# Kernel optimization log

Measured on AMD Instinct MI355X. Metric: run time of the kernel, lower is better.

The kernel has to match this reference:

```python
import jax, jax.numpy as jnp
import numpy as np

ENC_LEN, B, ENC2, DEC, E = 1024, 64, 1024, 512, 512

def setup_inputs() -> dict:
    key = jax.random.key(0)
    k1, k2, k3, k4 = jax.random.split(key, 4)
    enc_output = jax.random.normal(k1, (ENC_LEN, B, ENC2), dtype=jnp.float32)
    s = jax.random.normal(k2, (1, B, DEC), dtype=jnp.float32)
    # torch Linear weights: [out_features, in_features], no bias
    W_attn = jax.random.normal(k3, (E, ENC2 + DEC), dtype=jnp.float32) * (1.0 / np.sqrt(ENC2 + DEC))
    W_v = jax.random.normal(k4, (1, E), dtype=jnp.float32) * (1.0 / np.sqrt(E))
    return {"enc_output": enc_output, "s": s, "W_attn": W_attn, "W_v": W_v}

def reference(enc_output, s, W_attn, W_v):
    # cat([enc_output, s.repeat(L,1,1)], -1) @ W_attn.T  ==  enc @ Wa_e.T + s @ Wa_s.T (broadcast)
    enc2 = enc_output.shape[-1]
    Wa_e = W_attn[:, :enc2]          # [E, 2*enc_hid]
    Wa_s = W_attn[:, enc2:]          # [E, dec_hid]
    pre = jnp.einsum('lbc,ec->lbe', enc_output, Wa_e) + jnp.einsum('obd,ed->obe', s, Wa_s)
    engry = jnp.tanh(pre)            # [L, B, E]
    attention = jnp.einsum('lbe,oe->lbo', engry, W_v)[..., 0].T  # [B, L]
    return jax.nn.softmax(attention, axis=-1)
```

## Files before the change

### kernel.cpp

```cpp
#include <hip/hip_runtime.h>
#include <hip/hip_bf16.h>
#include <stdint.h>

typedef __bf16 bf16;
typedef __bf16 bf16x4 __attribute__((ext_vector_type(4)));
typedef __bf16 bf16x8 __attribute__((ext_vector_type(8)));
typedef float  f32x4  __attribute__((ext_vector_type(4)));

#define L_TOT 1024
#define B_TOT 64
#define C_TOT 1024
#define D_TOT 512
#define E_TOT 512
#define M_TOT (L_TOT * B_TOT)
#define W_LD  (C_TOT + D_TOT)

#define BM 128
#define BN 128
#define BK 32
#define NT 256
#define NKT (C_TOT / BK)

__device__ __forceinline__ void gload_lds16(const void* g, void* l) {
  __builtin_amdgcn_global_load_lds(
      (const __attribute__((address_space(1))) unsigned int*)(uintptr_t)g,
      (__attribute__((address_space(3))) unsigned int*)(uintptr_t)l,
      16, 0, 0);
}

__device__ __forceinline__ bf16x8 cvt8(f32x4 a, f32x4 b) {
  bf16x8 o;
  o[0]=(bf16)a[0]; o[1]=(bf16)a[1]; o[2]=(bf16)a[2]; o[3]=(bf16)a[3];
  o[4]=(bf16)b[0]; o[5]=(bf16)b[1]; o[6]=(bf16)b[2]; o[7]=(bf16)b[3];
  return o;
}

__device__ __forceinline__ float tanh_fast(float x) {
  float e = __expf(2.0f * x);
  return 1.0f - __fdividef(2.0f, e + 1.0f);
}

__global__ void convert_we_kernel(const float* __restrict__ Wattn,
                                  bf16* __restrict__ Wb) {
  const int e = blockIdx.x;
  const int t = threadIdx.x;
  const float4 v = ((const float4*)(Wattn + (size_t)e * W_LD))[t];
  bf16x4 o;
  o[0]=(bf16)v.x; o[1]=(bf16)v.y; o[2]=(bf16)v.z; o[3]=(bf16)v.w;
  ((bf16x4*)(Wb + (size_t)e * C_TOT))[t] = o;
}

__global__ void sb_kernel(const float* __restrict__ s,
                          const float* __restrict__ Wattn,
                          float* __restrict__ sb) {
  const int e = blockIdx.x;
  const int b = threadIdx.x;
  const float4* sr = (const float4*)(s + (size_t)b * D_TOT);
  const float4* wr = (const float4*)(Wattn + (size_t)e * W_LD + C_TOT);
  float acc = 0.f;
#pragma unroll 4
  for (int i = 0; i < D_TOT / 4; ++i) {
    float4 a = sr[i], w = wr[i];
    acc += a.x * w.x; acc += a.y * w.y; acc += a.z * w.z; acc += a.w * w.w;
  }
  sb[(size_t)b * E_TOT + e] = acc;
}

__global__ __launch_bounds__(NT, 4)
void gemm_tanh_dot_kernel(const float* __restrict__ A,
                          const bf16*  __restrict__ Wb,
                          const float* __restrict__ sb,
                          const float* __restrict__ Wv,
                          float* __restrict__ logitsQ) {
  __shared__ __align__(16) char smem[32768];
  char* const As0 = smem;
  char* const As1 = smem + 8192;
  char* const Bs0 = smem + 16384;
  char* const Bs1 = smem + 24576;

  const int tid  = threadIdx.x;
  const int lane = tid & 63;
  const int wid  = tid >> 6;
  const int wm   = wid >> 1;
  const int wn   = wid & 1;
  const int fr   = lane & 15;
  const int fg   = lane >> 4;

  const int blk = blockIdx.x;
  const int gx  = (blk & 7) | ((blk >> 5) << 3);
  const int gy  = (blk >> 3) & 3;
  const int m0  = gx << 7;
  const int e0  = gy << 7;

  const float* gA = A + (size_t)(m0 + (tid >> 1)) * C_TOT + ((tid & 1) << 4);
  const int ar  = tid >> 1;
  const int ap  = ar >> 1;
  const int as0 = ((ar & 1) << 2) | ((tid & 1) << 1);
  const int awo0 = ap * 128 + (((as0    ) ^ (ap & 7)) << 4);
  const int awo1 = ap * 128 + (((as0 + 1) ^ (ap & 7)) << 4);

  const int b_s = (tid & 7) ^ ((tid >> 3) & 7);
  const int b_r = ((tid >> 3) << 1) + (b_s >> 2);
  const bf16* gB = Wb + (size_t)(e0 + b_r) * C_TOT + ((b_s & 3) << 3);
  const int bdst = tid << 4;

  const int fxo = ((((fr & 1) << 2) | fg) ^ ((fr >> 1) & 7)) << 4;
  const int aro = ((wm << 5) + (fr >> 1)) * 128 + fxo;
  const int bro = ((wn << 5) + (fr >> 1)) * 128 + fxo;

  f32x4 acc[4][4];
#pragma unroll
  for (int i = 0; i < 4; ++i)
#pragma unroll
    for (int j = 0; j < 4; ++j)
      acc[i][j] = (f32x4){0.f, 0.f, 0.f, 0.f};

  f32x4 av00, av01, av02, av03, av10, av11, av12, av13;

  auto stageB = [&](char* Bp, int t) {
    const bf16* sp = gB + (t << 5);
    gload_lds16(sp,                        Bp + bdst);
    gload_lds16(sp + (size_t)64 * C_TOT,   Bp + bdst + 4096);
  };

#define LOADA(p, t)                                                            \
  { const float* ap_ = gA + ((t) << 5);                                        \
    asm volatile("global_load_dwordx4 %0, %1, off"           : "=v"(av##p##0) : "v"(ap_) : "memory"); \
    asm volatile("global_load_dwordx4 %0, %1, off offset:16" : "=v"(av##p##1) : "v"(ap_) : "memory"); \
    asm volatile("global_load_dwordx4 %0, %1, off offset:32" : "=v"(av##p##2) : "v"(ap_) : "memory"); \
    asm volatile("global_load_dwordx4 %0, %1, off offset:48" : "=v"(av##p##3) : "v"(ap_) : "memory"); }

#define WRITEA(Ap, p)                                                          \
  { *(bf16x8*)((Ap) + awo0) = cvt8(av##p##0, av##p##1);                        \
    *(bf16x8*)((Ap) + awo1) = cvt8(av##p##2, av##p##3); }

  auto phase = [&](const char* Ap, const char* Bp) {
    bf16x8 af[4], bf[4];
#pragma unroll
    for (int am = 0; am < 4; ++am) af[am] = *(const bf16x8*)(Ap + aro + am * 1024);
#pragma unroll
    for (int bn = 0; bn < 4; ++bn) bf[bn] = *(const bf16x8*)(Bp + bro + bn * 1024);
    __builtin_amdgcn_s_setprio(1);
#pragma unroll
    for (int am = 0; am < 4; ++am)
#pragma unroll
      for (int bn = 0; bn < 4; ++bn)
        acc[am][bn] = __builtin_amdgcn_mfma_f32_16x16x32_bf16(
            af[am], bf[bn], acc[am][bn], 0, 0, 0);
    __builtin_amdgcn_s_setprio(0);
  };

  stageB(Bs0, 0);
  LOADA(0, 0);
  asm volatile("s_waitcnt vmcnt(0)" ::: "memory");
  __builtin_amdgcn_sched_barrier(0);
  WRITEA(As0, 0);
  LOADA(1, 1);
  asm volatile("s_waitcnt lgkmcnt(0)" ::: "memory");
  __builtin_amdgcn_s_barrier();
  __builtin_amdgcn_sched_barrier(0);

#pragma unroll 1
  for (int kp = 0; kp < 15; ++kp) {
    const int t = kp << 1;
    stageB(Bs1, t + 1);
    LOADA(0, t + 2);
    asm volatile("s_waitcnt vmcnt(6)" ::: "memory");
    __builtin_amdgcn_sched_barrier(0);
    WRITEA(As1, 1);
    phase(As0, Bs0);
    asm volatile("s_waitcnt vmcnt(4) lgkmcnt(0)" ::: "memory");
    __builtin_amdgcn_s_barrier();
    __builtin_amdgcn_sched_barrier(0);
    stageB(Bs0, t + 2);
    LOADA(1, t + 3);
    asm volatile("s_waitcnt vmcnt(6)" ::: "memory");
    __builtin_amdgcn_sched_barrier(0);
    WRITEA(As0, 0);
    phase(As1, Bs1);
    asm volatile("s_waitcnt vmcnt(4) lgkmcnt(0)" ::: "memory");
    __builtin_amdgcn_s_barrier();
    __builtin_amdgcn_sched_barrier(0);
  }
  stageB(Bs1, 31);
  asm volatile("s_waitcnt vmcnt(2)" ::: "memory");
  __builtin_amdgcn_sched_barrier(0);
  WRITEA(As1, 1);
  phase(As0, Bs0);
  asm volatile("s_waitcnt vmcnt(0) lgkmcnt(0)" ::: "memory");
  __builtin_amdgcn_s_barrier();
  __builtin_amdgcn_sched_barrier(0);
  phase(As1, Bs1);

  float wv[4];
#pragma unroll
  for (int bn = 0; bn < 4; ++bn)
    wv[bn] = Wv[e0 + (wn << 6) + (bn << 4) + fr];

  float* red = (float*)smem;
#pragma unroll
  for (int am = 0; am < 4; ++am) {
#pragma unroll
    for (int j = 0; j < 4; ++j) {
      const int mloc = (wm << 6) + (am << 4) + (fg << 2) + j;
      const int bi = mloc & 63;
      const float* sbr = sb + (size_t)bi * E_TOT + e0 + (wn << 6) + fr;
      float c = 0.f;
#pragma unroll
      for (int bn = 0; bn < 4; ++bn)
        c += tanh_fast(acc[am][bn][j] + sbr[bn << 4]) * wv[bn];
      c += __shfl_xor(c, 1, 64);
      c += __shfl_xor(c, 2, 64);
      c += __shfl_xor(c, 4, 64);
      c += __shfl_xor(c, 8, 64);
      if (fr == 0) red[(wn << 7) + mloc] = c;
    }
  }
  __syncthreads();
  if (tid < BM)
    logitsQ[((size_t)gy << 16) + m0 + tid] = red[tid] + red[128 + tid];
#undef LOADA
#undef WRITEA
}

__global__ __launch_bounds__(256)
void softmax_kernel(const float* __restrict__ lQ, float* __restrict__ out) {
  const int b = blockIdx.x;
  const int t = threadIdx.x;
  const int lane = t & 63, w = t >> 6;
  __shared__ float sm[8];
  float x[4];
  float mx = -3.4e38f;
#pragma unroll
  for (int i = 0; i < 4; ++i) {
    const int m = (t + (i << 8)) * 64 + b;
    x[i] = (lQ[m] + lQ[(1 << 16) + m]) + (lQ[(2 << 16) + m] + lQ[(3 << 16) + m]);
    mx = fmaxf(mx, x[i]);
  }
#pragma unroll
  for (int off = 1; off < 64; off <<= 1)
    mx = fmaxf(mx, __shfl_xor(mx, off, 64));
  if (lane == 0) sm[w] = mx;
  __syncthreads();
  mx = fmaxf(fmaxf(sm[0], sm[1]), fmaxf(sm[2], sm[3]));
  float ex[4], ssum = 0.f;
#pragma unroll
  for (int i = 0; i < 4; ++i) { ex[i] = __expf(x[i] - mx); ssum += ex[i]; }
#pragma unroll
  for (int off = 1; off < 64; off <<= 1)
    ssum += __shfl_xor(ssum, off, 64);
  if (lane == 0) sm[4 + w] = ssum;
  __syncthreads();
  const float inv = 1.0f / (sm[4] + sm[5] + sm[6] + sm[7]);
#pragma unroll
  for (int i = 0; i < 4; ++i)
    out[(size_t)b * 1024 + t + (i << 8)] = ex[i] * inv;
}

extern "C" void kernel_launch(void* const* d_in, const int* in_sizes, int n_in,
                              void* d_out, int out_size, void* d_ws, size_t ws_size,
                              hipStream_t stream) {
  const float* enc = (const float*)d_in[0];
  const float* s   = (const float*)d_in[1];
  const float* Wat = (const float*)d_in[2];
  const float* Wv  = (const float*)d_in[3];
  float* out = (float*)d_out;

  char* ws = (char*)d_ws;
  bf16*  Wb      = (bf16*)ws;
  float* sb      = (float*)(ws + (1u << 20));
  float* logitsQ = (float*)(ws + (1u << 20) + (128u << 10));

  convert_we_kernel<<<E_TOT, 256, 0, stream>>>(Wat, Wb);
  sb_kernel<<<E_TOT, 64, 0, stream>>>(s, Wat, sb);
  gemm_tanh_dot_kernel<<<(M_TOT / BM) * 4, NT, 0, stream>>>(enc, Wb, sb, Wv, logitsQ);
  softmax_kernel<<<B_TOT, 256, 0, stream>>>(logitsQ, out);
}
```

Baseline: 160.8 us.

## Load GEMM operands directly from global into registers, removing LDS staging

Replaces the LDS double-buffered tile staging with direct per-lane global loads of MFMA fragments into registers, double-buffered in registers across k steps. Each wave now reads its own A and B fragments from global or cache, so data shared between waves is fetched repeatedly instead of once per block. This removes LDS writes and reads and the per-step barriers. In exchange it uses more registers, which is why occupancy is lowered to 2, and it relies on L1/L2 to absorb the repeated loads. The fp32 A fragments are read as strided 32-byte pieces per row, which may coalesce poorly.

```diff
diff --git a/kernel.cpp b/kernel.cpp
--- a/kernel.cpp
+++ b/kernel.cpp
@@ -15,18 +15,7 @@
 #define M_TOT (L_TOT * B_TOT)
 #define W_LD  (C_TOT + D_TOT)
 
-#define BM 128
-#define BN 128
-#define BK 32
 #define NT 256
-#define NKT (C_TOT / BK)
-
-__device__ __forceinline__ void gload_lds16(const void* g, void* l) {
-  __builtin_amdgcn_global_load_lds(
-      (const __attribute__((address_space(1))) unsigned int*)(uintptr_t)g,
-      (__attribute__((address_space(3))) unsigned int*)(uintptr_t)l,
-      16, 0, 0);
-}
 
 __device__ __forceinline__ bf16x8 cvt8(f32x4 a, f32x4 b) {
   bf16x8 o;
@@ -66,17 +55,13 @@
   sb[(size_t)b * E_TOT + e] = acc;
 }
 
-__global__ __launch_bounds__(NT, 4)
+__global__ __launch_bounds__(NT, 2)
 void gemm_tanh_dot_kernel(const float* __restrict__ A,
                           const bf16*  __restrict__ Wb,
                           const float* __restrict__ sb,
                           const float* __restrict__ Wv,
                           float* __restrict__ logitsQ) {
-  __shared__ __align__(16) char smem[32768];
-  char* const As0 = smem;
-  char* const As1 = smem + 8192;
-  char* const Bs0 = smem + 16384;
-  char* const Bs1 = smem + 24576;
+  __shared__ float red[512];
 
   const int tid  = threadIdx.x;
   const int lane = tid & 63;
@@ -92,21 +77,14 @@
   const int m0  = gx << 7;
   const int e0  = gy << 7;
 
-  const float* gA = A + (size_t)(m0 + (tid >> 1)) * C_TOT + ((tid & 1) << 4);
-  const int ar  = tid >> 1;
-  const int ap  = ar >> 1;
-  const int as0 = ((ar & 1) << 2) | ((tid & 1) << 1);
-  const int awo0 = ap * 128 + (((as0    ) ^ (ap & 7)) << 4);
-  const int awo1 = ap * 128 + (((as0 + 1) ^ (ap & 7)) << 4);
-
-  const int b_s = (tid & 7) ^ ((tid >> 3) & 7);
-  const int b_r = ((tid >> 3) << 1) + (b_s >> 2);
-  const bf16* gB = Wb + (size_t)(e0 + b_r) * C_TOT + ((b_s & 3) << 3);
-  const int bdst = tid << 4;
-
-  const int fxo = ((((fr & 1) << 2) | fg) ^ ((fr >> 1) & 7)) << 4;
-  const int aro = ((wm << 5) + (fr >> 1)) * 128 + fxo;
-  const int bro = ((wn << 5) + (fr >> 1)) * 128 + fxo;
+  const float* baseA[4];
+  const bf16*  baseB[4];
+#pragma unroll
+  for (int am = 0; am < 4; ++am)
+    baseA[am] = A + (size_t)(m0 + (wm << 6) + (am << 4) + fr) * C_TOT + (fg << 3);
+#pragma unroll
+  for (int bn = 0; bn < 4; ++bn)
+    baseB[bn] = Wb + (size_t)(e0 + (wn << 6) + (bn << 4) + fr) * C_TOT + (fg << 3);
 
   f32x4 acc[4][4];
 #pragma unroll
@@ -115,89 +93,51 @@
     for (int j = 0; j < 4; ++j)
       acc[i][j] = (f32x4){0.f, 0.f, 0.f, 0.f};
 
-  f32x4 av00, av01, av02, av03, av10, av11, av12, av13;
-
-  auto stageB = [&](char* Bp, int t) {
-    const bf16* sp = gB + (t << 5);
-    gload_lds16(sp,                        Bp + bdst);
-    gload_lds16(sp + (size_t)64 * C_TOT,   Bp + bdst + 4096);
+  f32x4  aS0[8], aS1[8];
+  bf16x8 bS0[4], bS1[4];
+
+  auto loadset = [&](f32x4* av, bf16x8* bv, int t) {
+    const int ko = t << 5;
+#pragma unroll
+    for (int am = 0; am < 4; ++am) {
+      av[2 * am]     = *(const f32x4*)(baseA[am] + ko);
+      av[2 * am + 1] = *(const f32x4*)(baseA[am] + ko + 4);
+    }
+#pragma unroll
+    for (int bn = 0; bn < 4; ++bn)
+      bv[bn] = *(const bf16x8*)(baseB[bn] + ko);
   };
 
-#define LOADA(p, t)                                                            \
-  { const float* ap_ = gA + ((t) << 5);                                        \
-    asm volatile("global_load_dwordx4 %0, %1, off"           : "=v"(av##p##0) : "v"(ap_) : "memory"); \
-    asm volatile("global_load_dwordx4 %0, %1, off offset:16" : "=v"(av##p##1) : "v"(ap_) : "memory"); \
-    asm volatile("global_load_dwordx4 %0, %1, off offset:32" : "=v"(av##p##2) : "v"(ap_) : "memory"); \
-    asm volatile("global_load_dwordx4 %0, %1, off offset:48" : "=v"(av##p##3) : "v"(ap_) : "memory"); }
-
-#define WRITEA(Ap, p)                                                          \
-  { *(bf16x8*)((Ap) + awo0) = cvt8(av##p##0, av##p##1);                        \
-    *(bf16x8*)((Ap) + awo1) = cvt8(av##p##2, av##p##3); }
-
-  auto phase = [&](const char* Ap, const char* Bp) {
-    bf16x8 af[4], bf[4];
-#pragma unroll
-    for (int am = 0; am < 4; ++am) af[am] = *(const bf16x8*)(Ap + aro + am * 1024);
-#pragma unroll
-    for (int bn = 0; bn < 4; ++bn) bf[bn] = *(const bf16x8*)(Bp + bro + bn * 1024);
+  auto computeset = [&](const f32x4* av, const bf16x8* bv) {
+    bf16x8 fa[4];
+#pragma unroll
+    for (int am = 0; am < 4; ++am)
+      fa[am] = cvt8(av[2 * am], av[2 * am + 1]);
     __builtin_amdgcn_s_setprio(1);
 #pragma unroll
     for (int am = 0; am < 4; ++am)
 #pragma unroll
       for (int bn = 0; bn < 4; ++bn)
         acc[am][bn] = __builtin_amdgcn_mfma_f32_16x16x32_bf16(
-            af[am], bf[bn], acc[am][bn], 0, 0, 0);
+            fa[am], bv[bn], acc[am][bn], 0, 0, 0);
     __builtin_amdgcn_s_setprio(0);
   };
 
-  stageB(Bs0, 0);
-  LOADA(0, 0);
-  asm volatile("s_waitcnt vmcnt(0)" ::: "memory");
-  __builtin_amdgcn_sched_barrier(0);
-  WRITEA(As0, 0);
-  LOADA(1, 1);
-  asm volatile("s_waitcnt lgkmcnt(0)" ::: "memory");
-  __builtin_amdgcn_s_barrier();
-  __builtin_amdgcn_sched_barrier(0);
-
+  loadset(aS0, bS0, 0);
 #pragma unroll 1
-  for (int kp = 0; kp < 15; ++kp) {
+  for (int kp = 0; kp < 16; ++kp) {
     const int t = kp << 1;
-    stageB(Bs1, t + 1);
-    LOADA(0, t + 2);
-    asm volatile("s_waitcnt vmcnt(6)" ::: "memory");
-    __builtin_amdgcn_sched_barrier(0);
-    WRITEA(As1, 1);
-    phase(As0, Bs0);
-    asm volatile("s_waitcnt vmcnt(4) lgkmcnt(0)" ::: "memory");
-    __builtin_amdgcn_s_barrier();
-    __builtin_amdgcn_sched_barrier(0);
-    stageB(Bs0, t + 2);
-    LOADA(1, t + 3);
-    asm volatile("s_waitcnt vmcnt(6)" ::: "memory");
-    __builtin_amdgcn_sched_barrier(0);
-    WRITEA(As0, 0);
-    phase(As1, Bs1);
-    asm volatile("s_waitcnt vmcnt(4) lgkmcnt(0)" ::: "memory");
-    __builtin_amdgcn_s_barrier();
-    __builtin_amdgcn_sched_barrier(0);
-  }
-  stageB(Bs1, 31);
-  asm volatile("s_waitcnt vmcnt(2)" ::: "memory");
-  __builtin_amdgcn_sched_barrier(0);
-  WRITEA(As1, 1);
-  phase(As0, Bs0);
-  asm volatile("s_waitcnt vmcnt(0) lgkmcnt(0)" ::: "memory");
-  __builtin_amdgcn_s_barrier();
-  __builtin_amdgcn_sched_barrier(0);
-  phase(As1, Bs1);
+    loadset(aS1, bS1, t + 1);
+    computeset(aS0, bS0);
+    if (kp < 15) loadset(aS0, bS0, t + 2);
+    computeset(aS1, bS1);
+  }
 
   float wv[4];
 #pragma unroll
   for (int bn = 0; bn < 4; ++bn)
     wv[bn] = Wv[e0 + (wn << 6) + (bn << 4) + fr];
 
-  float* red = (float*)smem;
 #pragma unroll
   for (int am = 0; am < 4; ++am) {
 #pragma unroll
@@ -217,10 +157,8 @@
     }
   }
   __syncthreads();
-  if (tid < BM)
+  if (tid < 128)
     logitsQ[((size_t)gy << 16) + m0 + tid] = red[tid] + red[128 + tid];
-#undef LOADA
-#undef WRITEA
 }
 
 __global__ __launch_bounds__(256)
@@ -273,6 +211,6 @@
 
   convert_we_kernel<<<E_TOT, 256, 0, stream>>>(Wat, Wb);
   sb_kernel<<<E_TOT, 64, 0, stream>>>(s, Wat, sb);
-  gemm_tanh_dot_kernel<<<(M_TOT / BM) * 4, NT, 0, stream>>>(enc, Wb, sb, Wv, logitsQ);
+  gemm_tanh_dot_kernel<<<512 * 4, NT, 0, stream>>>(enc, Wb, sb, Wv, logitsQ);
   softmax_kernel<<<B_TOT, 256, 0, stream>>>(logitsQ, out);
 }
```

New measurement: 384.1 us. 2.39x slower.
